# Optimization experiments

Hardware: AMD Instinct MI355X
Metric: run time of the kernel (lower is better)

Reference implementation:

```python
import jax, jax.numpy as jnp
import numpy as np

EMBED_DIM = 1024
NUM_HEADS = 16
HEAD_DIM = EMBED_DIM // NUM_HEADS
EPSILON = 1e-6
SCORE_SCALE = 1.0
B, L = 2, 2048


def setup_inputs() -> dict:
    key = jax.random.key(0)
    k0, k1, k2, k3, k4 = jax.random.split(key, 5)
    s_in = 1.0 / np.sqrt(EMBED_DIM)
    return {
        "x": jax.random.normal(k0, (B, L, EMBED_DIM), dtype=jnp.float32),
        "w_qkv": jax.random.normal(k1, (EMBED_DIM, 3 * EMBED_DIM), dtype=jnp.float32) * s_in,
        "b_qkv": jnp.zeros((3 * EMBED_DIM,), dtype=jnp.float32),
        "w_out": jax.random.normal(k2, (EMBED_DIM, EMBED_DIM), dtype=jnp.float32) * s_in,
        "b_out": jnp.zeros((EMBED_DIM,), dtype=jnp.float32),
    }


def reference(x, w_qkv, b_qkv, w_out, b_out):
    Bq, Lq, E = x.shape
    qkv = x @ w_qkv + b_qkv  # [B, L, 3E]
    q, k, v = jnp.split(qkv, 3, axis=-1)
    q = q.reshape(Bq, Lq, NUM_HEADS, HEAD_DIM).transpose(0, 2, 1, 3)  # bhld
    k = k.reshape(Bq, Lq, NUM_HEADS, HEAD_DIM).transpose(0, 2, 1, 3)
    v = v.reshape(Bq, Lq, NUM_HEADS, HEAD_DIM).transpose(0, 2, 1, 3)

    dot = jnp.einsum('bhid,bhjd->bhij', q, k)
    q_norm_sq = jnp.sum(q * q, axis=-1, keepdims=True)          # [b,h,L,1]
    k_norm_sq = jnp.sum(k * k, axis=-1, keepdims=True)          # [b,h,L,1]
    vals = q_norm_sq + k_norm_sq.transpose(0, 1, 3, 2)          # [b,h,L,L]
    scores = (dot * dot) / (vals - 2.0 * dot + EPSILON) * SCORE_SCALE

    mask = jnp.triu(jnp.ones((Lq, Lq), dtype=scores.dtype), k=1) * -1e9
    scores = scores + mask[None, None, :, :]
    attn = jax.nn.softmax(scores, axis=-1)
    out = jnp.einsum('bhij,bhjd->bhid', attn, v)
    out = out.transpose(0, 2, 1, 3).reshape(Bq, Lq, E)
    return out @ w_out + b_out
```

## Files before the change

### kernel.cpp

```cpp
#include <hip/hip_runtime.h>

#define EMBED 1024
#define NH 16
#define HD 64
#define SEQ 2048
#define BATCH 2
#define ROWS (BATCH*SEQ)
#define BHD (BATCH*NH)

typedef __bf16 bf16x8 __attribute__((ext_vector_type(8)));
typedef _Float16 f16x4 __attribute__((ext_vector_type(4)));
typedef float f32x4 __attribute__((ext_vector_type(4)));

__device__ __forceinline__ unsigned short f2bf(float f){
  union { float f; unsigned u; } v; v.f = f;
  unsigned r = v.u + 0x7fffu + ((v.u >> 16) & 1u);
  return (unsigned short)(r >> 16);
}
__device__ __forceinline__ float bf2f(unsigned short s){
  union { unsigned u; float f; } v; v.u = ((unsigned)s) << 16; return v.f;
}
__device__ __forceinline__ unsigned short f2h(float f){
  union { _Float16 h; unsigned short u; } v; v.h = (_Float16)f; return v.u;
}

typedef __attribute__((address_space(1))) unsigned int as1_t;
typedef __attribute__((address_space(3))) unsigned int as3_t;
__device__ __forceinline__ void async_ld16(const void* gp, void* lp){
  __builtin_amdgcn_global_load_lds((as1_t*)gp, (as3_t*)lp, 16, 0, 0);
}


__global__ __launch_bounds__(256) void k_conv(const float* __restrict__ x,
                                              unsigned short* __restrict__ xb, int n4){
  int i = blockIdx.x * blockDim.x + threadIdx.x;
  if (i < n4){
    float4 f = ((const float4*)x)[i];
    ushort4 o;
    o.x = f2bf(f.x); o.y = f2bf(f.y); o.z = f2bf(f.z); o.w = f2bf(f.w);
    ((ushort4*)xb)[i] = o;
  }
}

__global__ __launch_bounds__(256) void k_tr_f2b(const float* __restrict__ in,
                                                unsigned short* __restrict__ out, int R, int C){
  __shared__ float t[32][33];
  int c0 = blockIdx.x * 32, r0 = blockIdx.y * 32;
  int tx = threadIdx.x, ty = threadIdx.y;
  #pragma unroll
  for (int i = 0; i < 4; i++){ int r = ty + i*8; t[r][tx] = in[(size_t)(r0+r)*C + c0 + tx]; }
  __syncthreads();
  #pragma unroll
  for (int i = 0; i < 4; i++){ int rr = ty + i*8; out[(size_t)(c0+rr)*R + r0 + tx] = f2bf(t[tx][rr]); }
}

__global__ __launch_bounds__(256) void k_tr_b2b(const unsigned short* __restrict__ in,
                                                unsigned short* __restrict__ out, int R, int C){
  in  += (size_t)blockIdx.z * R * C;
  out += (size_t)blockIdx.z * R * C;
  __shared__ unsigned short t[32][33];
  int c0 = blockIdx.x * 32, r0 = blockIdx.y * 32;
  int tx = threadIdx.x, ty = threadIdx.y;
  #pragma unroll
  for (int i = 0; i < 4; i++){ int r = ty + i*8; t[r][tx] = in[(size_t)(r0+r)*C + c0 + tx]; }
  __syncthreads();
  #pragma unroll
  for (int i = 0; i < 4; i++){ int rr = ty + i*8; out[(size_t)(c0+rr)*R + r0 + tx] = t[tx][rr]; }
}

__global__ __launch_bounds__(256) void k_norms(const unsigned short* __restrict__ q,
                                               const unsigned short* __restrict__ k,
                                               float* __restrict__ qn, float* __restrict__ kn){
  int i = blockIdx.x * blockDim.x + threadIdx.x;
  const uint4* qr = (const uint4*)(q + (size_t)i * HD);
  const uint4* kr = (const uint4*)(k + (size_t)i * HD);
  float sq = 0.f, sk = 0.f;
  #pragma unroll
  for (int t = 0; t < 8; t++){
    uint4 uq = qr[t], uk = kr[t];
    unsigned aq[4] = {uq.x, uq.y, uq.z, uq.w};
    unsigned ak[4] = {uk.x, uk.y, uk.z, uk.w};
    #pragma unroll
    for (int j = 0; j < 4; j++){
      float f0 = bf2f((unsigned short)(aq[j] & 0xffff));
      float f1 = bf2f((unsigned short)(aq[j] >> 16));
      sq += f0*f0 + f1*f1;
      float g0 = bf2f((unsigned short)(ak[j] & 0xffff));
      float g1 = bf2f((unsigned short)(ak[j] >> 16));
      sk += g0*g0 + g1*g1;
    }
  }
  qn[i] = sq; kn[i] = sk;
}


__global__ __launch_bounds__(256) void k_gemm_qkv(
    const unsigned short* __restrict__ A,
    const unsigned short* __restrict__ BT,
    const float* __restrict__ bias,
    unsigned short* __restrict__ qo, unsigned short* __restrict__ ko,
    unsigned short* __restrict__ vo)
{
  __shared__ __align__(16) unsigned short As[128*32];
  __shared__ __align__(16) unsigned short Bs[128*32];
  const int K = EMBED;
  int m0 = blockIdx.x * 128, n0 = blockIdx.y * 128;
  int tid = threadIdx.x, lane = tid & 63, wave = tid >> 6;
  int wm = wave >> 1, wn = wave & 1;
  int l16 = lane & 15, quad = lane >> 4;
  f32x4 acc[4][4] = {};
  int c0i = wave*64 + lane, c1i = 256 + wave*64 + lane;
  int r0 = c0i >> 2, cc0 = (c0i & 3) * 8;
  int r1 = c1i >> 2, cc1 = (c1i & 3) * 8;
  unsigned short* lA0 = &As[(wave*64)*8];
  unsigned short* lA1 = &As[(256 + wave*64)*8];
  unsigned short* lB0 = &Bs[(wave*64)*8];
  unsigned short* lB1 = &Bs[(256 + wave*64)*8];
  for (int k0 = 0; k0 < K; k0 += 32){
    async_ld16((void*)&A [(size_t)(m0 + r0)*K + k0 + cc0], (void*)lA0);
    async_ld16((void*)&A [(size_t)(m0 + r1)*K + k0 + cc1], (void*)lA1);
    async_ld16((void*)&BT[(size_t)(n0 + r0)*K + k0 + cc0], (void*)lB0);
    async_ld16((void*)&BT[(size_t)(n0 + r1)*K + k0 + cc1], (void*)lB1);
    __syncthreads();
    bf16x8 af[4], bfr[4];
    #pragma unroll
    for (int mi = 0; mi < 4; mi++) af[mi]  = *(const bf16x8*)&As[(wm*64 + mi*16 + l16)*32 + quad*8];
    #pragma unroll
    for (int ni = 0; ni < 4; ni++) bfr[ni] = *(const bf16x8*)&Bs[(wn*64 + ni*16 + l16)*32 + quad*8];
    #pragma unroll
    for (int mi = 0; mi < 4; mi++)
      #pragma unroll
      for (int ni = 0; ni < 4; ni++)
        acc[mi][ni] = __builtin_amdgcn_mfma_f32_16x16x32_bf16(af[mi], bfr[ni], acc[mi][ni], 0, 0, 0);
    __syncthreads();
  }
  #pragma unroll
  for (int mi = 0; mi < 4; mi++)
    #pragma unroll
    for (int ni = 0; ni < 4; ni++)
      #pragma unroll
      for (int rr = 0; rr < 4; rr++){
        int row = m0 + wm*64 + mi*16 + quad*4 + rr;
        int col = n0 + wn*64 + ni*16 + l16;
        float val = acc[mi][ni][rr] + bias[col];
        int b = row >> 11, l = row & 2047;
        int which = col >> 10, e = col & 1023, h = e >> 6, d = e & 63;
        unsigned short* dst = which == 0 ? qo : (which == 1 ? ko : vo);
        unsigned short bits = (which == 2) ? f2h(val) : f2bf(val);
        dst[(((size_t)(b*NH + h))*SEQ + l)*HD + d] = bits;
      }
}


__global__ __launch_bounds__(128, 4) void k_attn(
    const unsigned short* __restrict__ qg,
    const unsigned short* __restrict__ kg,
    const unsigned short* __restrict__ vtg,
    const float* __restrict__ qn,
    const float* __restrict__ kn,
    float* __restrict__ Opart,
    float* __restrict__ Mp,
    float* __restrict__ Lp)
{
  __shared__ __align__(16) unsigned short Ks[2][32*72];
  __shared__ __align__(16) _Float16      Vs[2][64*36];
  int bh = blockIdx.y;
  int tid = threadIdx.x, lane = tid & 63, wave = tid >> 6;
  int l16 = lane & 15, quad = lane >> 4;
  int P = blockIdx.x >> 1, s = blockIdx.x & 1;

  const unsigned short* qbase = qg  + (size_t)bh * SEQ * HD;
  const unsigned short* kbase = kg  + (size_t)bh * SEQ * HD;
  const _Float16*       vtb   = (const _Float16*)vtg + (size_t)bh * HD * SEQ;
  const float* knb = kn + (size_t)bh * SEQ;

  int kd0 = tid >> 3,         kc0 = tid & 7;
  int kd1 = (tid + 128) >> 3, kc1 = tid & 7;
  int vd0 = tid >> 2,         vc0 = tid & 3;
  int vd1 = 32 + (tid >> 2),  vc1 = tid & 3;

  #pragma unroll
  for (int pass = 0; pass < 2; pass++){
    int t = pass ? (63 - P) : P;
    int nj = t + 1;
    int half = (nj + 1) >> 1;
    int jb_lo = s ? half : 0;
    int jb_hi = s ? nj : half;
    int q0 = t*32 + wave*16;

    bf16x8 aq[2];
    #pragma unroll
    for (int sk = 0; sk < 2; sk++)
      aq[sk] = *(const bf16x8*)&qbase[(size_t)(q0 + l16)*HD + sk*32 + quad*8];
    float qn_m = qn[(size_t)bh*SEQ + q0 + l16];

    float m_run = -1e30f, l_lane = 0.f;
    f32x4 oacc[4] = {};

    if (jb_lo < jb_hi){
      int jlo = jb_lo * 32;
      {
        uint4 ka = *(const uint4*)&kbase[(size_t)(jlo + kd0)*HD + kc0*8];
        uint4 kb = *(const uint4*)&kbase[(size_t)(jlo + kd1)*HD + kc1*8];
        uint4 va = *(const uint4*)&vtb[(size_t)vd0*SEQ + jlo + vc0*8];
        uint4 vb = *(const uint4*)&vtb[(size_t)vd1*SEQ + jlo + vc1*8];
        *(uint4*)&Ks[0][kd0*72 + kc0*8] = ka;
        *(uint4*)&Ks[0][kd1*72 + kc1*8] = kb;
        *(uint2*)&Vs[0][vd0*36 + vc0*8]     = make_uint2(va.x, va.y);
        *(uint2*)&Vs[0][vd0*36 + vc0*8 + 4] = make_uint2(va.z, va.w);
        *(uint2*)&Vs[0][vd1*36 + vc1*8]     = make_uint2(vb.x, vb.y);
        *(uint2*)&Vs[0][vd1*36 + vc1*8 + 4] = make_uint2(vb.z, vb.w);
      }
      __syncthreads();

      for (int jb = jb_lo; jb < jb_hi; jb++){
        int j0 = jb * 32;
        int buf = (jb - jb_lo) & 1;
        int jn = (jb + 1 < jb_hi) ? (jb + 1)*32 : j0;
        uint4 ka = *(const uint4*)&kbase[(size_t)(jn + kd0)*HD + kc0*8];
        uint4 kb = *(const uint4*)&kbase[(size_t)(jn + kd1)*HD + kc1*8];
        uint4 va = *(const uint4*)&vtb[(size_t)vd0*SEQ + jn + vc0*8];
        uint4 vb = *(const uint4*)&vtb[(size_t)vd1*SEQ + jn + vc1*8];

        f32x4 st[2] = {};
        #pragma unroll
        for (int tile = 0; tile < 2; tile++)
          #pragma unroll
          for (int sk = 0; sk < 2; sk++){
            bf16x8 ak = *(const bf16x8*)&Ks[buf][(tile*16 + l16)*72 + (sk*4 + quad)*8];
            st[tile] = __builtin_amdgcn_mfma_f32_16x16x32_bf16(ak, aq[sk], st[tile], 0, 0, 0);
          }
        float4 kn_a = *(const float4*)&knb[j0 + quad*4];
        float4 kn_b = *(const float4*)&knb[j0 + 16 + quad*4];
        float kn_j[2][4] = {{kn_a.x, kn_a.y, kn_a.z, kn_a.w}, {kn_b.x, kn_b.y, kn_b.z, kn_b.w}};
        int mg = q0 + l16;
        float sc[2][4];
        if (j0 + 32 > q0){
          #pragma unroll
          for (int tile = 0; tile < 2; tile++)
            #pragma unroll
            for (int rr = 0; rr < 4; rr++){
              int jg = j0 + tile*16 + quad*4 + rr;
              float dot = st[tile][rr];
              float den = fmaxf(qn_m + kn_j[tile][rr] - 2.0f*dot, 0.0f) + 1e-6f;
              float v = dot * dot * __builtin_amdgcn_rcpf(den);
              sc[tile][rr] = (jg <= mg) ? v : -1e30f;
            }
        } else {
          #pragma unroll
          for (int tile = 0; tile < 2; tile++)
            #pragma unroll
            for (int rr = 0; rr < 4; rr++){
              float dot = st[tile][rr];
              float den = fmaxf(qn_m + kn_j[tile][rr] - 2.0f*dot, 0.0f) + 1e-6f;
              sc[tile][rr] = dot * dot * __builtin_amdgcn_rcpf(den);
            }
        }
        float mx = fmaxf(fmaxf(fmaxf(sc[0][0], sc[0][1]), fmaxf(sc[0][2], sc[0][3])),
                         fmaxf(fmaxf(sc[1][0], sc[1][1]), fmaxf(sc[1][2], sc[1][3])));
        mx = fmaxf(mx, __shfl_xor(mx, 16));
        mx = fmaxf(mx, __shfl_xor(mx, 32));
        float mnew = fmaxf(m_run, mx);
        float alpha = __expf(m_run - mnew);
        m_run = mnew;

        float ps = 0.f;
        #pragma unroll
        for (int tile = 0; tile < 2; tile++)
          #pragma unroll
          for (int rr = 0; rr < 4; rr++){
            float e = __expf(sc[tile][rr] - mnew);
            sc[tile][rr] = e; ps += e;
          }
        l_lane = l_lane * alpha + ps;

        #pragma unroll
        for (int g = 0; g < 4; g++)
          #pragma unroll
          for (int rr = 0; rr < 4; rr++) oacc[g][rr] *= alpha;

        #pragma unroll
        for (int tile = 0; tile < 2; tile++){
          f16x4 pf;
          #pragma unroll
          for (int rr = 0; rr < 4; rr++) pf[rr] = (_Float16)sc[tile][rr];
          #pragma unroll
          for (int g = 0; g < 4; g++){
            f16x4 av = *(const f16x4*)&Vs[buf][(g*16 + l16)*36 + (tile*4 + quad)*4];
            oacc[g] = __builtin_amdgcn_mfma_f32_16x16x16f16(av, pf, oacc[g], 0, 0, 0);
          }
        }

        *(uint4*)&Ks[buf^1][kd0*72 + kc0*8] = ka;
        *(uint4*)&Ks[buf^1][kd1*72 + kc1*8] = kb;
        *(uint2*)&Vs[buf^1][vd0*36 + vc0*8]     = make_uint2(va.x, va.y);
        *(uint2*)&Vs[buf^1][vd0*36 + vc0*8 + 4] = make_uint2(va.z, va.w);
        *(uint2*)&Vs[buf^1][vd1*36 + vc1*8]     = make_uint2(vb.x, vb.y);
        *(uint2*)&Vs[buf^1][vd1*36 + vc1*8 + 4] = make_uint2(vb.z, vb.w);
        __syncthreads();
      }
    }

    float l_tot = l_lane + __shfl_xor(l_lane, 16);
    l_tot += __shfl_xor(l_tot, 32);

    int r = wave*16 + l16;
    size_t pb = ((size_t)(bh*64 + t)*2 + s) * (32*64);
    #pragma unroll
    for (int g = 0; g < 4; g++){
      float4 pk = make_float4(oacc[g][0], oacc[g][1], oacc[g][2], oacc[g][3]);
      *(float4*)&Opart[pb + (size_t)r*64 + g*16 + quad*4] = pk;
    }
    if (quad == 0){
      int mb = ((bh*64 + t)*2 + s)*32 + r;
      Mp[mb] = m_run;
      Lp[mb] = l_tot;
    }
    __syncthreads();
  }
}


__global__ __launch_bounds__(256) void k_combine(
    const float* __restrict__ Opart,
    const float* __restrict__ Mp,
    const float* __restrict__ Lp,
    unsigned short* __restrict__ attn_out)
{
  int t = blockIdx.x;
  int bh = blockIdx.y; int b = bh >> 4, h = bh & 15;
  int tid = threadIdx.x;
  int d = tid & 63, r8 = (tid >> 6) * 8;
  size_t i0 = ((size_t)(bh*64 + t)*2) * 2048;
  size_t i1 = i0 + 2048;
  int mb = ((bh*64 + t)*2) * 32;
  #pragma unroll
  for (int rr = 0; rr < 8; rr++){
    int r = r8 + rr;
    float m0 = Mp[mb + r],      m1 = Mp[mb + 32 + r];
    float l0 = Lp[mb + r],      l1 = Lp[mb + 32 + r];
    float ms = fmaxf(m0, m1);
    float w0 = __expf(m0 - ms), w1 = __expf(m1 - ms);
    float den = w0*l0 + w1*l1;
    float o = (w0*Opart[i0 + (size_t)r*64 + d] + w1*Opart[i1 + (size_t)r*64 + d]) / den;
    attn_out[(size_t)(b*SEQ + t*32 + r)*EMBED + h*HD + d] = f2bf(o);
  }
}


__global__ __launch_bounds__(256) void k_gemm_out(
    const unsigned short* __restrict__ A,
    const unsigned short* __restrict__ BT,
    const float* __restrict__ bias,
    float* __restrict__ out)
{
  __shared__ __align__(16) unsigned short As[128*32];
  __shared__ __align__(16) unsigned short Bs[128*32];
  const int K = EMBED;
  int m0 = blockIdx.x * 128, n0 = blockIdx.y * 128;
  int tid = threadIdx.x, lane = tid & 63, wave = tid >> 6;
  int wm = wave >> 1, wn = wave & 1;
  int l16 = lane & 15, quad = lane >> 4;
  f32x4 acc[4][4] = {};
  int c0i = wave*64 + lane, c1i = 256 + wave*64 + lane;
  int r0 = c0i >> 2, cc0 = (c0i & 3) * 8;
  int r1 = c1i >> 2, cc1 = (c1i & 3) * 8;
  unsigned short* lA0 = &As[(wave*64)*8];
  unsigned short* lA1 = &As[(256 + wave*64)*8];
  unsigned short* lB0 = &Bs[(wave*64)*8];
  unsigned short* lB1 = &Bs[(256 + wave*64)*8];
  for (int k0 = 0; k0 < K; k0 += 32){
    async_ld16((void*)&A [(size_t)(m0 + r0)*K + k0 + cc0], (void*)lA0);
    async_ld16((void*)&A [(size_t)(m0 + r1)*K + k0 + cc1], (void*)lA1);
    async_ld16((void*)&BT[(size_t)(n0 + r0)*K + k0 + cc0], (void*)lB0);
    async_ld16((void*)&BT[(size_t)(n0 + r1)*K + k0 + cc1], (void*)lB1);
    __syncthreads();
    bf16x8 af[4], bfr[4];
    #pragma unroll
    for (int mi = 0; mi < 4; mi++) af[mi]  = *(const bf16x8*)&As[(wm*64 + mi*16 + l16)*32 + quad*8];
    #pragma unroll
    for (int ni = 0; ni < 4; ni++) bfr[ni] = *(const bf16x8*)&Bs[(wn*64 + ni*16 + l16)*32 + quad*8];
    #pragma unroll
    for (int mi = 0; mi < 4; mi++)
      #pragma unroll
      for (int ni = 0; ni < 4; ni++)
        acc[mi][ni] = __builtin_amdgcn_mfma_f32_16x16x32_bf16(af[mi], bfr[ni], acc[mi][ni], 0, 0, 0);
    __syncthreads();
  }
  #pragma unroll
  for (int mi = 0; mi < 4; mi++)
    #pragma unroll
    for (int ni = 0; ni < 4; ni++)
      #pragma unroll
      for (int rr = 0; rr < 4; rr++){
        int row = m0 + wm*64 + mi*16 + quad*4 + rr;
        int col = n0 + wn*64 + ni*16 + l16;
        out[(size_t)row*EMBED + col] = acc[mi][ni][rr] + bias[col];
      }
}


extern "C" void kernel_launch(void* const* d_in, const int* in_sizes, int n_in,
                              void* d_out, int out_size, void* d_ws, size_t ws_size,
                              hipStream_t stream) {
  const float* x     = (const float*)d_in[0];
  const float* w_qkv = (const float*)d_in[1];
  const float* b_qkv = (const float*)d_in[2];
  const float* w_out = (const float*)d_in[3];
  const float* b_out = (const float*)d_in[4];
  float* out = (float*)d_out;

  char* ws = (char*)d_ws;
  size_t off = 0;
  auto alloc = [&](size_t bytes) -> void* {
    void* p = ws + off; off += (bytes + 255) & ~(size_t)255; return p;
  };
  unsigned short* xb    = (unsigned short*)alloc((size_t)ROWS * EMBED * 2);
  unsigned short* wqkvT = (unsigned short*)alloc((size_t)3 * EMBED * EMBED * 2);
  unsigned short* woutT = (unsigned short*)alloc((size_t)EMBED * EMBED * 2);
  unsigned short* qb    = (unsigned short*)alloc((size_t)ROWS * EMBED * 2);
  unsigned short* kb    = (unsigned short*)alloc((size_t)ROWS * EMBED * 2);
  unsigned short* vb    = (unsigned short*)alloc((size_t)ROWS * EMBED * 2);
  unsigned short* vTb   = (unsigned short*)alloc((size_t)ROWS * EMBED * 2);
  float* qn = (float*)alloc((size_t)BHD * SEQ * 4);
  float* kn = (float*)alloc((size_t)BHD * SEQ * 4);
  float* Opart = (float*)alloc((size_t)BHD * 64 * 2 * 32 * 64 * 4);
  float* Mp    = (float*)alloc((size_t)BHD * 64 * 2 * 32 * 4);
  float* Lp    = (float*)alloc((size_t)BHD * 64 * 2 * 32 * 4);
  unsigned short* attnb = xb;

  k_conv<<<dim3((ROWS*EMBED/4 + 255)/256), dim3(256), 0, stream>>>(x, xb, ROWS*EMBED/4);
  k_tr_f2b<<<dim3(3*EMBED/32, EMBED/32), dim3(32, 8), 0, stream>>>(w_qkv, wqkvT, EMBED, 3*EMBED);
  k_tr_f2b<<<dim3(EMBED/32, EMBED/32), dim3(32, 8), 0, stream>>>(w_out, woutT, EMBED, EMBED);
  k_gemm_qkv<<<dim3(ROWS/128, 3*EMBED/128), dim3(256), 0, stream>>>(xb, wqkvT, b_qkv, qb, kb, vb);
  k_norms<<<dim3(BHD*SEQ/256), dim3(256), 0, stream>>>(qb, kb, qn, kn);
  k_tr_b2b<<<dim3(HD/32, SEQ/32, BHD), dim3(32, 8), 0, stream>>>(vb, vTb, SEQ, HD);
  k_attn<<<dim3(64, BHD), dim3(128), 0, stream>>>(qb, kb, vTb, qn, kn, Opart, Mp, Lp);
  k_combine<<<dim3(64, BHD), dim3(256), 0, stream>>>(Opart, Mp, Lp, attnb);
  k_gemm_out<<<dim3(ROWS/128, EMBED/128), dim3(256), 0, stream>>>(attnb, woutT, b_out, out);
}
```

Before: 222.4 us.

## Fuse prep kernels and fold norms and V transpose into QKV GEMM epilogue

Merges the x conversion and both weight transposes into one prep kernel. The QKV GEMM epilogue now computes the q/k squared norms with wave shuffles and writes V already transposed. This drops the separate norms and V-transpose kernels, their launches, and a full extra read and write of q, k and v. The trade-off is a heavier GEMM epilogue, with transposed V stores that are strided across SEQ.

Measured after the change: 222.4 us. About the same (+0.0%).

```diff
diff --git a/kernel.cpp b/kernel.cpp
--- a/kernel.cpp
+++ b/kernel.cpp
@@ -31,22 +31,32 @@
 }
 
 
-__global__ __launch_bounds__(256) void k_conv(const float* __restrict__ x,
-                                              unsigned short* __restrict__ xb, int n4){
-  int i = blockIdx.x * blockDim.x + threadIdx.x;
-  if (i < n4){
+__global__ __launch_bounds__(256) void k_prep(
+    const float* __restrict__ x,     unsigned short* __restrict__ xb,
+    const float* __restrict__ wqkv,  unsigned short* __restrict__ wqkvT,
+    const float* __restrict__ wout,  unsigned short* __restrict__ woutT)
+{
+  __shared__ float t[32][33];
+  int tid = threadIdx.x;
+  int bx = blockIdx.x;
+  if (bx < 4096){
+    int i = bx*256 + tid;
     float4 f = ((const float4*)x)[i];
-    ushort4 o;
-    o.x = f2bf(f.x); o.y = f2bf(f.y); o.z = f2bf(f.z); o.w = f2bf(f.w);
+    ushort4 o; o.x=f2bf(f.x); o.y=f2bf(f.y); o.z=f2bf(f.z); o.w=f2bf(f.w);
     ((ushort4*)xb)[i] = o;
-  }
-}
-
-__global__ __launch_bounds__(256) void k_tr_f2b(const float* __restrict__ in,
-                                                unsigned short* __restrict__ out, int R, int C){
-  __shared__ float t[32][33];
-  int c0 = blockIdx.x * 32, r0 = blockIdx.y * 32;
-  int tx = threadIdx.x, ty = threadIdx.y;
+    return;
+  }
+  const float* in; unsigned short* out; int R, C, c0, r0;
+  if (bx < 4096 + 3072){
+    int bid = bx - 4096;
+    in = wqkv; out = wqkvT; R = 1024; C = 3072;
+    c0 = (bid % 96) * 32; r0 = (bid / 96) * 32;
+  } else {
+    int bid = bx - 7168;
+    in = wout; out = woutT; R = 1024; C = 1024;
+    c0 = (bid & 31) * 32; r0 = (bid >> 5) * 32;
+  }
+  int tx = tid & 31, ty = tid >> 5;
   #pragma unroll
   for (int i = 0; i < 4; i++){ int r = ty + i*8; t[r][tx] = in[(size_t)(r0+r)*C + c0 + tx]; }
   __syncthreads();
@@ -54,52 +64,14 @@
   for (int i = 0; i < 4; i++){ int rr = ty + i*8; out[(size_t)(c0+rr)*R + r0 + tx] = f2bf(t[tx][rr]); }
 }
 
-__global__ __launch_bounds__(256) void k_tr_b2b(const unsigned short* __restrict__ in,
-                                                unsigned short* __restrict__ out, int R, int C){
-  in  += (size_t)blockIdx.z * R * C;
-  out += (size_t)blockIdx.z * R * C;
-  __shared__ unsigned short t[32][33];
-  int c0 = blockIdx.x * 32, r0 = blockIdx.y * 32;
-  int tx = threadIdx.x, ty = threadIdx.y;
-  #pragma unroll
-  for (int i = 0; i < 4; i++){ int r = ty + i*8; t[r][tx] = in[(size_t)(r0+r)*C + c0 + tx]; }
-  __syncthreads();
-  #pragma unroll
-  for (int i = 0; i < 4; i++){ int rr = ty + i*8; out[(size_t)(c0+rr)*R + r0 + tx] = t[tx][rr]; }
-}
-
-__global__ __launch_bounds__(256) void k_norms(const unsigned short* __restrict__ q,
-                                               const unsigned short* __restrict__ k,
-                                               float* __restrict__ qn, float* __restrict__ kn){
-  int i = blockIdx.x * blockDim.x + threadIdx.x;
-  const uint4* qr = (const uint4*)(q + (size_t)i * HD);
-  const uint4* kr = (const uint4*)(k + (size_t)i * HD);
-  float sq = 0.f, sk = 0.f;
-  #pragma unroll
-  for (int t = 0; t < 8; t++){
-    uint4 uq = qr[t], uk = kr[t];
-    unsigned aq[4] = {uq.x, uq.y, uq.z, uq.w};
-    unsigned ak[4] = {uk.x, uk.y, uk.z, uk.w};
-    #pragma unroll
-    for (int j = 0; j < 4; j++){
-      float f0 = bf2f((unsigned short)(aq[j] & 0xffff));
-      float f1 = bf2f((unsigned short)(aq[j] >> 16));
-      sq += f0*f0 + f1*f1;
-      float g0 = bf2f((unsigned short)(ak[j] & 0xffff));
-      float g1 = bf2f((unsigned short)(ak[j] >> 16));
-      sk += g0*g0 + g1*g1;
-    }
-  }
-  qn[i] = sq; kn[i] = sk;
-}
-
 
 __global__ __launch_bounds__(256) void k_gemm_qkv(
     const unsigned short* __restrict__ A,
     const unsigned short* __restrict__ BT,
     const float* __restrict__ bias,
     unsigned short* __restrict__ qo, unsigned short* __restrict__ ko,
-    unsigned short* __restrict__ vo)
+    unsigned short* __restrict__ vT,
+    float* __restrict__ qn, float* __restrict__ kn)
 {
   __shared__ __align__(16) unsigned short As[128*32];
   __shared__ __align__(16) unsigned short Bs[128*32];
@@ -134,21 +106,54 @@
         acc[mi][ni] = __builtin_amdgcn_mfma_f32_16x16x32_bf16(af[mi], bfr[ni], acc[mi][ni], 0, 0, 0);
     __syncthreads();
   }
-  #pragma unroll
-  for (int mi = 0; mi < 4; mi++)
-    #pragma unroll
-    for (int ni = 0; ni < 4; ni++)
+
+  int which = n0 >> 10;
+  int h = ((n0 & 1023) >> 6) + wn;
+  if (which < 2){
+    unsigned short* dst = (which == 0) ? qo : ko;
+    float* ndst = (which == 0) ? qn : kn;
+    #pragma unroll
+    for (int mi = 0; mi < 4; mi++){
+      float ns[4] = {0.f, 0.f, 0.f, 0.f};
+      #pragma unroll
+      for (int ni = 0; ni < 4; ni++)
+        #pragma unroll
+        for (int rr = 0; rr < 4; rr++){
+          int row = m0 + wm*64 + mi*16 + quad*4 + rr;
+          int col = n0 + wn*64 + ni*16 + l16;
+          unsigned short bits = f2bf(acc[mi][ni][rr] + bias[col]);
+          int b = row >> 11, l = row & 2047;
+          dst[(((size_t)(b*NH + h))*SEQ + l)*HD + (col & 63)] = bits;
+          float vq = bf2f(bits);
+          ns[rr] += vq * vq;
+        }
       #pragma unroll
       for (int rr = 0; rr < 4; rr++){
-        int row = m0 + wm*64 + mi*16 + quad*4 + rr;
+        float s = ns[rr];
+        s += __shfl_xor(s, 1); s += __shfl_xor(s, 2);
+        s += __shfl_xor(s, 4); s += __shfl_xor(s, 8);
+        if (l16 == 0){
+          int row = m0 + wm*64 + mi*16 + quad*4 + rr;
+          int b = row >> 11, l = row & 2047;
+          ndst[(size_t)(b*NH + h)*SEQ + l] = s;
+        }
+      }
+    }
+  } else {
+    #pragma unroll
+    for (int mi = 0; mi < 4; mi++)
+      #pragma unroll
+      for (int ni = 0; ni < 4; ni++){
+        int row0 = m0 + wm*64 + mi*16 + quad*4;
         int col = n0 + wn*64 + ni*16 + l16;
-        float val = acc[mi][ni][rr] + bias[col];
-        int b = row >> 11, l = row & 2047;
-        int which = col >> 10, e = col & 1023, h = e >> 6, d = e & 63;
-        unsigned short* dst = which == 0 ? qo : (which == 1 ? ko : vo);
-        unsigned short bits = (which == 2) ? f2h(val) : f2bf(val);
-        dst[(((size_t)(b*NH + h))*SEQ + l)*HD + d] = bits;
+        int b = row0 >> 11, l0 = row0 & 2047;
+        ushort4 pk; unsigned short* pks = (unsigned short*)&pk;
+        #pragma unroll
+        for (int rr = 0; rr < 4; rr++)
+          pks[rr] = f2h(acc[mi][ni][rr] + bias[col]);
+        *(ushort4*)&vT[(((size_t)(b*NH + h))*HD + (col & 63))*SEQ + l0] = pk;
       }
+  }
 }
 
 
@@ -420,7 +425,6 @@
   unsigned short* woutT = (unsigned short*)alloc((size_t)EMBED * EMBED * 2);
   unsigned short* qb    = (unsigned short*)alloc((size_t)ROWS * EMBED * 2);
   unsigned short* kb    = (unsigned short*)alloc((size_t)ROWS * EMBED * 2);
-  unsigned short* vb    = (unsigned short*)alloc((size_t)ROWS * EMBED * 2);
   unsigned short* vTb   = (unsigned short*)alloc((size_t)ROWS * EMBED * 2);
   float* qn = (float*)alloc((size_t)BHD * SEQ * 4);
   float* kn = (float*)alloc((size_t)BHD * SEQ * 4);
@@ -429,12 +433,8 @@
   float* Lp    = (float*)alloc((size_t)BHD * 64 * 2 * 32 * 4);
   unsigned short* attnb = xb;
 
-  k_conv<<<dim3((ROWS*EMBED/4 + 255)/256), dim3(256), 0, stream>>>(x, xb, ROWS*EMBED/4);
-  k_tr_f2b<<<dim3(3*EMBED/32, EMBED/32), dim3(32, 8), 0, stream>>>(w_qkv, wqkvT, EMBED, 3*EMBED);
-  k_tr_f2b<<<dim3(EMBED/32, EMBED/32), dim3(32, 8), 0, stream>>>(w_out, woutT, EMBED, EMBED);
-  k_gemm_qkv<<<dim3(ROWS/128, 3*EMBED/128), dim3(256), 0, stream>>>(xb, wqkvT, b_qkv, qb, kb, vb);
-  k_norms<<<dim3(BHD*SEQ/256), dim3(256), 0, stream>>>(qb, kb, qn, kn);
-  k_tr_b2b<<<dim3(HD/32, SEQ/32, BHD), dim3(32, 8), 0, stream>>>(vb, vTb, SEQ, HD);
+  k_prep<<<dim3(4096 + 3072 + 1024), dim3(256), 0, stream>>>(x, xb, w_qkv, wqkvT, w_out, woutT);
+  k_gemm_qkv<<<dim3(ROWS/128, 3*EMBED/128), dim3(256), 0, stream>>>(xb, wqkvT, b_qkv, qb, kb, vTb, qn, kn);
   k_attn<<<dim3(64, BHD), dim3(128), 0, stream>>>(qb, kb, vTb, qn, kn, Opart, Mp, Lp);
   k_combine<<<dim3(64, BHD), dim3(256), 0, stream>>>(Opart, Mp, Lp, attnb);
   k_gemm_out<<<dim3(ROWS/128, EMBED/128), dim3(256), 0, stream>>>(attnb, woutT, b_out, out);
```
